# Kernel tuning notes

Measured on AMD Instinct MI355X. Metric: run time of the kernel, lower is better.

Reference implementation:

```python
import jax, jax.numpy as jnp
import numpy as np

B, T_AUDIO, D_IN = 64, 500, 768
H = 1024
NUM_CHARS = 1024  # must equal H: one-hot char embeddings feed the LSTM input
SEQ_LEN = 128


def setup_inputs() -> dict:
    key = jax.random.key(0)
    ks = jax.random.split(key, 16)
    s = 1.0 / np.sqrt(H)
    u = lambda k, shape: jax.random.uniform(k, shape, jnp.float32, -s, s)
    return {
        "audio_features": jax.random.normal(ks[0], (B, T_AUDIO, D_IN), jnp.float32),
        "text_indices": jax.random.randint(ks[1], (B, SEQ_LEN), 0, NUM_CHARS),
        "W_proj": u(ks[2], (H, D_IN)), "b_proj": u(ks[3], (H,)),
        "W_ih0": u(ks[4], (4 * H, H)), "W_hh0": u(ks[5], (4 * H, H)),
        "b_ih0": u(ks[6], (4 * H,)), "b_hh0": u(ks[7], (4 * H,)),
        "W_ih1": u(ks[8], (4 * H, H)), "W_hh1": u(ks[9], (4 * H, H)),
        "b_ih1": u(ks[10], (4 * H,)), "b_hh1": u(ks[11], (4 * H,)),
        "W_out": u(ks[12], (NUM_CHARS, H)), "b_out": u(ks[13], (NUM_CHARS,)),
    }


def _lstm_cell(x, h, c, W_ih, W_hh, b_ih, b_hh):
    # PyTorch gate order: i, f, g, o
    g = x @ W_ih.T + h @ W_hh.T + b_ih + b_hh
    i, f, gg, o = jnp.split(g, 4, axis=-1)
    c = jax.nn.sigmoid(f) * c + jax.nn.sigmoid(i) * jnp.tanh(gg)
    h = jax.nn.sigmoid(o) * jnp.tanh(c)
    return h, c


def reference(audio_features, text_indices, W_proj, b_proj,
              W_ih0, W_hh0, b_ih0, b_hh0,
              W_ih1, W_hh1, b_ih1, b_hh1,
              W_out, b_out):
    # audio encoding: project then mean-pool over time -> [B, H]
    audio_enc = jnp.mean(audio_features @ W_proj.T + b_proj, axis=1)
    seq_len = text_indices.shape[1]
    # teacher-forcing inputs: step 0 = audio encoding, steps 1..L-1 = one-hot of
    # text_indices[:, 1:seq_len-1] (NUM_CHARS == H)
    one_hots = jax.nn.one_hot(text_indices[:, 1:seq_len - 1], NUM_CHARS,
                              dtype=audio_enc.dtype)  # [B, L-1, H]
    xs = jnp.concatenate([audio_enc[:, None, :], one_hots], axis=1)  # [B, L, H]
    xs = jnp.swapaxes(xs, 0, 1)  # [L, B, H]
    z = jnp.zeros((audio_enc.shape[0], H), audio_enc.dtype)

    def step(carry, x):
        h0, c0, h1, c1 = carry
        h0, c0 = _lstm_cell(x, h0, c0, W_ih0, W_hh0, b_ih0, b_hh0)
        h1, c1 = _lstm_cell(h0, h1, c1, W_ih1, W_hh1, b_ih1, b_hh1)
        return (h0, c0, h1, c1), h1

    _, hs = jax.lax.scan(step, (z, z, z, z), xs)  # hs: [L, B, H]
    outs = jnp.swapaxes(hs, 0, 1)  # [B, L, H]
    logits = outs @ W_out.T + b_out  # [B, L, NUM_CHARS]
    return logits
```

## Files before the change

### kernel.cpp

```cpp
#include <hip/hip_runtime.h>
#include <hip/hip_bf16.h>

#define HH     1024
#define BB     64
#define DIN    768
#define TAUD   500
#define LSTEPS 127
#define G4     4096
#define NB     256
#define BHH    (BB*HH)

typedef __attribute__((ext_vector_type(8))) short bf16x8;
typedef __attribute__((ext_vector_type(4))) float f32x4;
typedef unsigned short u16;
typedef unsigned long long u64;

__device__ __forceinline__ u16 f2b(float x){
  __hip_bfloat16 h = __float2bfloat16(x);
  return __builtin_bit_cast(u16, h);
}
__device__ __forceinline__ float b2f(u16 u){
  unsigned int x = ((unsigned int)u) << 16;
  return __builtin_bit_cast(float, x);
}
__device__ __forceinline__ float sig_(float x){ return 1.0f/(1.0f+__expf(-x)); }
__device__ __forceinline__ float tanh_(float x){
  float ax = fabsf(x);
  float e  = __expf(-2.0f*ax);
  float t  = (1.0f-e)/(1.0f+e);
  return x < 0.0f ? -t : t;
}

constexpr size_t O_PACK  = 0;
constexpr size_t O_WG    = O_PACK + (size_t)NB*3*16384*2;
constexpr size_t O_WOHI  = O_WG   + (size_t)NB*16384*2;
constexpr size_t O_WOLO  = O_WOHI + (size_t)HH*HH*2;
constexpr size_t O_B0P   = O_WOLO + (size_t)HH*HH*2;
constexpr size_t O_B1P   = O_B0P  + G4*4;
constexpr size_t O_G0    = O_B1P  + G4*4;
constexpr size_t O_MEAN  = O_G0   + (size_t)BB*HH*4*4;
constexpr size_t O_X0    = O_MEAN + (size_t)BB*DIN*4;
constexpr size_t O_H0    = O_X0   + (size_t)BHH*2;
constexpr size_t O_H1    = O_H0   + (size_t)2*BHH*2;
constexpr size_t O_HS    = O_H1   + (size_t)2*BHH*2;
constexpr size_t O_BAR   = O_HS   + (size_t)LSTEPS*BHH*2;

__global__ void init_kernel(u16* h0, u16* h1, int* bar){
  int i = blockIdx.x*256 + threadIdx.x;
  int st = gridDim.x*256;
  for (int k=i;k<2*BHH;k+=st){ h0[k]=0; h1[k]=0; }
  if (i < 512) bar[i] = 0;
}

__global__ void pool_kernel(const float* __restrict__ audio, float* __restrict__ mean){
  int b = blockIdx.x/3, dc = blockIdx.x%3;
  int d = dc*256 + threadIdx.x;
  const float* p = audio + (size_t)b*TAUD*DIN + d;
  float s = 0.f;
  #pragma unroll 5
  for (int t=0;t<TAUD;++t) s += p[(size_t)t*DIN];
  mean[b*DIN + d] = s*(1.0f/TAUD);
}

__global__ void project_kernel(const float* __restrict__ mean, const float* __restrict__ Wp,
                               const float* __restrict__ bp, u16* __restrict__ x0){
  __shared__ float wrow[DIN];
  __shared__ float part[256];
  int h = blockIdx.x;
  for (int i=threadIdx.x;i<DIN;i+=256) wrow[i] = Wp[(size_t)h*DIN + i];
  __syncthreads();
  int b = threadIdx.x>>2, q = threadIdx.x&3;
  const float* mr = mean + b*DIN + q*192;
  const float* wr = wrow + q*192;
  float s = 0.f;
  #pragma unroll 8
  for (int i=0;i<192;++i) s += mr[i]*wr[i];
  part[threadIdx.x] = s;
  __syncthreads();
  if (q==0){
    float v = part[threadIdx.x]+part[threadIdx.x+1]+part[threadIdx.x+2]+part[threadIdx.x+3] + bp[h];
    x0[b*HH + h] = f2b(v);
  }
}

__global__ void g0_kernel(const float* __restrict__ Wih0, const u16* __restrict__ x0bf,
                          float* __restrict__ G0p){
  __shared__ float wr[4][HH];
  __shared__ float part[256][4];
  int u = blockIdx.x;
  for (int i=threadIdx.x; i<4*HH; i+=256){
    int g = i>>10, k = i&1023;
    wr[g][k] = b2f(f2b(Wih0[(size_t)(u + g*HH)*HH + k]));
  }
  __syncthreads();
  int b = threadIdx.x>>2, q = threadIdx.x&3;
  const u16* xr = x0bf + b*HH + q*256;
  float s0=0,s1=0,s2=0,s3=0;
  for (int k=0;k<256;++k){
    float xv = b2f(xr[k]);
    s0 += xv*wr[0][q*256+k]; s1 += xv*wr[1][q*256+k];
    s2 += xv*wr[2][q*256+k]; s3 += xv*wr[3][q*256+k];
  }
  part[threadIdx.x][0]=s0; part[threadIdx.x][1]=s1;
  part[threadIdx.x][2]=s2; part[threadIdx.x][3]=s3;
  __syncthreads();
  if (threadIdx.x < 64){
    int bb = threadIdx.x;
    #pragma unroll
    for (int g=0;g<4;++g){
      float v = part[bb*4][g]+part[bb*4+1][g]+part[bb*4+2][g]+part[bb*4+3][g];
      G0p[((size_t)bb*HH + u)*4 + g] = v;
    }
  }
}

__global__ void pack_w_kernel(const float* __restrict__ Whh0, const float* __restrict__ Wih1,
                              const float* __restrict__ Whh1, u16* __restrict__ P){
  int bid = blockIdx.x, m = blockIdx.y;
  const float* src = (m==0)? Whh0 : (m==1)? Wih1 : Whh1;
  u16* dst = P + ((size_t)bid*3 + m)*16384;
  for (int e = threadIdx.x; e < 16384; e += 256){
    int r = e&31, col = (e>>5)&15, ktg = e>>9;
    int ng = bid*4 + (col&3) + (col>>2)*HH;
    dst[e] = f2b(src[(size_t)ng*HH + ktg*32 + r]);
  }
}

__global__ void pack_wg_kernel(const float* __restrict__ Wih0, u16* __restrict__ WG){
  int bid = blockIdx.x;
  for (int i = threadIdx.x; i < 16384; i += 256){
    int ch = i>>4, u = (i>>2)&3, g = i&3;
    WG[(size_t)bid*16384 + i] = f2b(Wih0[(size_t)(bid*4 + u + g*HH)*HH + ch]);
  }
}

__global__ void pack_bias_kernel(const float* bih0, const float* bhh0,
                                 const float* bih1, const float* bhh1,
                                 float* B0p, float* B1p){
  int i = blockIdx.x*256 + threadIdx.x;
  if (i < G4){
    int n = (i>>2) + (i&3)*HH;
    B0p[i] = bih0[n]+bhh0[n];
    B1p[i] = bih1[n]+bhh1[n];
  }
}

__global__ void wout_kernel(const float* __restrict__ src, u16* __restrict__ hi,
                            u16* __restrict__ lo, int n){
  int i = blockIdx.x*256+threadIdx.x, st = gridDim.x*256;
  for (;i<n;i+=st){
    float v = src[i];
    u16 h = f2b(v);
    hi[i] = h;
    lo[i] = f2b(v - b2f(h));
  }
}

__device__ __forceinline__ void sysst32(unsigned* p, unsigned v){
  __hip_atomic_store(p, v, __ATOMIC_RELAXED, __HIP_MEMORY_SCOPE_SYSTEM);
}

__device__ __forceinline__ void gridbar(int* bar, int t){
  __syncthreads();
  if (threadIdx.x==0){
    int leaf = blockIdx.x>>4;
    int a = __hip_atomic_fetch_add(&bar[leaf*32], 1, __ATOMIC_RELAXED, __HIP_MEMORY_SCOPE_SYSTEM);
    int r = a - t*16;
    if (r == 15)
      __hip_atomic_fetch_add(&bar[511], 1, __ATOMIC_RELAXED, __HIP_MEMORY_SCOPE_SYSTEM);
    if (r == 0 || r == 15){
      while (__hip_atomic_load(&bar[511], __ATOMIC_RELAXED, __HIP_MEMORY_SCOPE_SYSTEM) < (t+1)*16)
        __builtin_amdgcn_s_sleep(4);
      if (r == 0)
        __hip_atomic_store(&bar[leaf*32+16], t+1, __ATOMIC_RELAXED, __HIP_MEMORY_SCOPE_SYSTEM);
    } else {
      while (__hip_atomic_load(&bar[leaf*32+16], __ATOMIC_RELAXED, __HIP_MEMORY_SCOPE_SYSTEM) < t+1)
        __builtin_amdgcn_s_sleep(4);
    }
    asm volatile("" ::: "memory");
  }
  __syncthreads();
  if (threadIdx.x < 64)
    __builtin_amdgcn_fence(__ATOMIC_ACQUIRE, "agent");
  __syncthreads();
}

__device__ __forceinline__ f32x4 gemmK(const u16* __restrict__ A, const u16* B, f32x4 acc){
  #pragma unroll
  for (int h=0; h<2; ++h){
    bf16x8 af[16];
    #pragma unroll
    for (int i=0;i<16;++i) af[i] = *(const bf16x8*)(A + (h*16+i)*32);
    #pragma unroll
    for (int i=0;i<16;++i)
      acc = __builtin_amdgcn_mfma_f32_16x16x32_bf16(af[i], *(const bf16x8*)(B + (h*16+i)*512), acc, 0,0,0);
  }
  return acc;
}
__device__ __forceinline__ f32x4 gemm2K(const u16* __restrict__ A1, const u16* __restrict__ A2,
                                        const u16* B1, const u16* B2){
  f32x4 a1 = {0,0,0,0}, a2 = {0,0,0,0};
  #pragma unroll
  for (int h=0; h<2; ++h){
    bf16x8 af[16], ag[16];
    #pragma unroll
    for (int i=0;i<16;++i) af[i] = *(const bf16x8*)(A1 + (h*16+i)*32);
    #pragma unroll
    for (int i=0;i<16;++i) ag[i] = *(const bf16x8*)(A2 + (h*16+i)*32);
    #pragma unroll
    for (int i=0;i<16;++i){
      a1 = __builtin_amdgcn_mfma_f32_16x16x32_bf16(af[i], *(const bf16x8*)(B1 + (h*16+i)*512), a1, 0,0,0);
      a2 = __builtin_amdgcn_mfma_f32_16x16x32_bf16(ag[i], *(const bf16x8*)(B2 + (h*16+i)*512), a2, 0,0,0);
    }
  }
  return a1 + a2;
}

__device__ __forceinline__ void xpose(const f32x4 acc, float* gv, int lane){
  const int base = lane & 48, up = (lane>>2)&3, r = lane&3;
  #pragma unroll
  for (int g=0; g<4; ++g){
    int src = base | (g*4 + up);
    float v0 = __shfl(acc[0], src);
    float v1 = __shfl(acc[1], src);
    float v2 = __shfl(acc[2], src);
    float v3 = __shfl(acc[3], src);
    gv[g] = (r==0)? v0 : (r==1)? v1 : (r==2)? v2 : v3;
  }
}

__global__ void __launch_bounds__(256, 1) lstm_kernel(
    const u16* __restrict__ P, const u16* __restrict__ WG,
    const float* __restrict__ B0p, const float* __restrict__ B1p,
    const float* __restrict__ G0p, const int* __restrict__ tix,
    u16* __restrict__ h0bf, u16* __restrict__ h1bf,
    u16* __restrict__ hs, int* __restrict__ bar)
{
  extern __shared__ char smem[];
  u16* Plds = (u16*)smem;
  u16* WGl  = (u16*)(smem + 98304);
  u16* tixl = (u16*)(smem + 98304 + 32768);

  const int tid  = threadIdx.x;
  const int lane = tid&63, mg = tid>>6, quad = lane>>4, colc = lane&15;
  const int bid  = blockIdx.x;

  {
    const bf16x8* gs = (const bf16x8*)(P + (size_t)bid*49152);
    bf16x8* gd = (bf16x8*)Plds;
    #pragma unroll
    for (int i=0;i<24;++i) gd[tid + i*256] = gs[tid + i*256];
    const bf16x8* ws = (const bf16x8*)(WG + (size_t)bid*16384);
    bf16x8* wd = (bf16x8*)WGl;
    #pragma unroll
    for (int i=0;i<8;++i) wd[tid + i*256] = ws[tid + i*256];
    for (int i=tid; i<BB*128; i+=256) tixl[i] = (u16)tix[(i&63)*128 + (i>>6)];
  }

  const int aoff = (mg*16 + colc)*HH + quad*8;
  const int boff = colc*32 + quad*8;
  const u16* B_hh0 = Plds + boff;
  const u16* B_ih1 = Plds + 16384 + boff;
  const u16* B_hh1 = Plds + 2*16384 + boff;

  const int bT = mg*16 + quad*4 + (lane&3);
  const int up = (lane>>2)&3;
  const int ug = bid*4 + up;
  const float4 vb0 = *(const float4*)(B0p + ug*4);
  const float4 vb1 = *(const float4*)(B1p + ug*4);
  float cc0 = 0.f, cc1 = 0.f;
  __syncthreads();

  {
    float4 g0 = *(const float4*)(G0p + ((size_t)bT*HH + ug)*4);
    float gi = g0.x+vb0.x, gf = g0.y+vb0.y, gg = g0.z+vb0.z, go = g0.w+vb0.w;
    cc0 = sig_(gi)*tanh_(gg);
    unsigned hv = f2b(sig_(go)*tanh_(cc0));
    unsigned ov = __shfl_xor(hv, 4);
    if ((lane&4)==0)
      sysst32((unsigned*)(h0bf + (size_t)BHH) + (bT*HH + ug)/2, hv | (ov<<16));
  }

  #pragma unroll 1
  for (int t=0;t<LSTEPS;++t){
    const int cur = t&1, nxt = cur^1;
    gridbar(bar, t);
    {
      f32x4 acc = gemm2K(h0bf + (size_t)nxt*BHH + aoff, h1bf + (size_t)cur*BHH + aoff,
                         B_ih1, B_hh1);
      float gv[4];
      xpose(acc, gv, lane);
      gv[0]+=vb1.x; gv[1]+=vb1.y; gv[2]+=vb1.z; gv[3]+=vb1.w;
      cc1 = sig_(gv[1])*cc1 + sig_(gv[0])*tanh_(gv[2]);
      unsigned hv = f2b(sig_(gv[3])*tanh_(cc1));
      unsigned ov = __shfl_xor(hv, 4);
      if ((lane&4)==0){
        unsigned pk = hv | (ov<<16);
        sysst32((unsigned*)(h1bf + (size_t)nxt*BHH) + (bT*HH + ug)/2, pk);
        sysst32((unsigned*)hs + (((size_t)t*BB + bT)*HH + ug)/2, pk);
      }
    }
    if (t < LSTEPS-1){
      f32x4 z = {0,0,0,0};
      f32x4 acc = gemmK(h0bf + (size_t)nxt*BHH + aoff, B_hh0, z);
      float gv[4];
      xpose(acc, gv, lane);
      int ch = tixl[(t+1)*64 + bT];
      ushort4 wv = *(const ushort4*)(WGl + ch*16 + up*4);
      gv[0]+=vb0.x+b2f(wv.x); gv[1]+=vb0.y+b2f(wv.y);
      gv[2]+=vb0.z+b2f(wv.z); gv[3]+=vb0.w+b2f(wv.w);
      cc0 = sig_(gv[1])*cc0 + sig_(gv[0])*tanh_(gv[2]);
      unsigned hv = f2b(sig_(gv[3])*tanh_(cc0));
      unsigned ov = __shfl_xor(hv, 4);
      if ((lane&4)==0)
        sysst32((unsigned*)(h0bf + (size_t)cur*BHH) + (bT*HH + ug)/2, hv | (ov<<16));
    }
  }
}

__global__ void __launch_bounds__(512) logits_kernel(
    const u16* __restrict__ hs, const u16* __restrict__ Whi, const u16* __restrict__ Wlo,
    const float* __restrict__ bout, float* __restrict__ out)
{
  extern __shared__ u16 bsh[];
  const int tid = threadIdx.x;
  const int w = tid>>6, lane = tid&63, quad = lane>>4, col = lane&15;
  const int mt = blockIdx.x*8 + w;
  const bool active = (mt < (LSTEPS*BB)/16);
  bf16x8 afr[32];
  if (active){
    const u16* ap = hs + (size_t)(mt*16+col)*HH + quad*8;
    #pragma unroll
    for (int kt=0;kt<32;++kt) afr[kt] = *(const bf16x8*)(ap + kt*32);
  }
  const int nt0 = blockIdx.y*16;
  for (int nt=nt0; nt<nt0+16; ++nt){
    __syncthreads();
    #pragma unroll
    for (int i=0;i<8;++i){
      int cid = i*512 + tid;
      int mat = cid>>11;
      int r = (cid>>7)&15, ck = cid&127;
      const u16* src = (mat? Wlo : Whi) + (size_t)(nt*16+r)*HH + ck*8;
      *(bf16x8*)(bsh + mat*16512 + r*1032 + ck*8) = *(const bf16x8*)src;
    }
    __syncthreads();
    if (active){
      f32x4 acc = {0.f,0.f,0.f,0.f};
      const u16* bh = bsh + col*1032 + quad*8;
      const u16* bl = bsh + 16512 + col*1032 + quad*8;
      #pragma unroll 8
      for (int kt=0;kt<32;++kt){
        bf16x8 b1 = *(const bf16x8*)(bh + kt*32);
        acc = __builtin_amdgcn_mfma_f32_16x16x32_bf16(afr[kt], b1, acc, 0,0,0);
        bf16x8 b2 = *(const bf16x8*)(bl + kt*32);
        acc = __builtin_amdgcn_mfma_f32_16x16x32_bf16(afr[kt], b2, acc, 0,0,0);
      }
      float bb = bout[nt*16 + col];
      #pragma unroll
      for (int r=0;r<4;++r){
        int m = mt*16 + quad*4 + r;
        int tt = m>>6, b_ = m&63;
        out[((size_t)b_*LSTEPS + tt)*HH + nt*16 + col] = acc[r] + bb;
      }
    }
  }
}

extern "C" void kernel_launch(void* const* d_in, const int* in_sizes, int n_in,
                              void* d_out, int out_size, void* d_ws, size_t ws_size,
                              hipStream_t stream) {
  const float* audio = (const float*)d_in[0];
  const int*   tix   = (const int*)  d_in[1];
  const float* Wproj = (const float*)d_in[2];
  const float* bproj = (const float*)d_in[3];
  const float* Wih0  = (const float*)d_in[4];
  const float* Whh0  = (const float*)d_in[5];
  const float* bih0  = (const float*)d_in[6];
  const float* bhh0  = (const float*)d_in[7];
  const float* Wih1  = (const float*)d_in[8];
  const float* Whh1  = (const float*)d_in[9];
  const float* bih1  = (const float*)d_in[10];
  const float* bhh1  = (const float*)d_in[11];
  const float* Wout  = (const float*)d_in[12];
  const float* bout  = (const float*)d_in[13];
  float* out = (float*)d_out;

  char* ws = (char*)d_ws;
  u16*   wP    = (u16*)  (ws + O_PACK);
  u16*   wWG   = (u16*)  (ws + O_WG);
  u16*   wWoHi = (u16*)  (ws + O_WOHI);
  u16*   wWoLo = (u16*)  (ws + O_WOLO);
  float* wB0p  = (float*)(ws + O_B0P);
  float* wB1p  = (float*)(ws + O_B1P);
  float* wG0   = (float*)(ws + O_G0);
  float* wMean = (float*)(ws + O_MEAN);
  u16*   wX0   = (u16*)  (ws + O_X0);
  u16*   wH0   = (u16*)  (ws + O_H0);
  u16*   wH1   = (u16*)  (ws + O_H1);
  u16*   wHS   = (u16*)  (ws + O_HS);
  int*   wBar  = (int*)  (ws + O_BAR);

  init_kernel<<<64, 256, 0, stream>>>(wH0, wH1, wBar);
  pool_kernel<<<BB*3, 256, 0, stream>>>(audio, wMean);
  project_kernel<<<HH, 256, 0, stream>>>(wMean, Wproj, bproj, wX0);
  g0_kernel<<<HH, 256, 0, stream>>>(Wih0, wX0, wG0);
  pack_w_kernel<<<dim3(NB,3), 256, 0, stream>>>(Whh0, Wih1, Whh1, wP);
  pack_wg_kernel<<<NB, 256, 0, stream>>>(Wih0, wWG);
  pack_bias_kernel<<<16, 256, 0, stream>>>(bih0, bhh0, bih1, bhh1, wB0p, wB1p);
  wout_kernel<<<512, 256, 0, stream>>>(Wout, wWoHi, wWoLo, HH*HH);
  lstm_kernel<<<NB, 256, 98304 + 32768 + 16384, stream>>>(
      wP, wWG, wB0p, wB1p, wG0, tix, wH0, wH1, wHS, wBar);
  logits_kernel<<<dim3(64,4), 512, 66048, stream>>>(wHS, wWoHi, wWoLo, bout, out);
}
```

Measured before the change: 2.625 ms.

## Use never-reused per-step hidden-state buffers and drop acquire fence from grid barrier

Replaces the double-buffered h0/h1 ping-pong with a full per-timestep history for h0, and reads h1 straight from the hs output history. Because each address is written only once, the acquire fence after the grid barrier is removed on the assumption that stale cache lines cannot exist. The zero-init of the hidden buffers is no longer needed, and step 0 skips the h1 recurrent GEMM. This uses more workspace memory. Correctness now depends on never-written addresses not being held in non-coherent caches without a fence.

```diff
diff --git a/kernel.cpp b/kernel.cpp
--- a/kernel.cpp
+++ b/kernel.cpp
@@ -40,16 +40,12 @@
 constexpr size_t O_G0    = O_B1P  + G4*4;
 constexpr size_t O_MEAN  = O_G0   + (size_t)BB*HH*4*4;
 constexpr size_t O_X0    = O_MEAN + (size_t)BB*DIN*4;
-constexpr size_t O_H0    = O_X0   + (size_t)BHH*2;
-constexpr size_t O_H1    = O_H0   + (size_t)2*BHH*2;
-constexpr size_t O_HS    = O_H1   + (size_t)2*BHH*2;
+constexpr size_t O_H0R   = O_X0   + (size_t)BHH*2;
+constexpr size_t O_HS    = O_H0R  + (size_t)LSTEPS*BHH*2;
 constexpr size_t O_BAR   = O_HS   + (size_t)LSTEPS*BHH*2;
 
-__global__ void init_kernel(u16* h0, u16* h1, int* bar){
-  int i = blockIdx.x*256 + threadIdx.x;
-  int st = gridDim.x*256;
-  for (int k=i;k<2*BHH;k+=st){ h0[k]=0; h1[k]=0; }
-  if (i < 512) bar[i] = 0;
+__global__ void init_kernel(int* bar){
+  if (threadIdx.x < 512) bar[threadIdx.x] = 0;
 }
 
 __global__ void pool_kernel(const float* __restrict__ audio, float* __restrict__ mean){
@@ -180,9 +176,6 @@
     asm volatile("" ::: "memory");
   }
   __syncthreads();
-  if (threadIdx.x < 64)
-    __builtin_amdgcn_fence(__ATOMIC_ACQUIRE, "agent");
-  __syncthreads();
 }
 
 __device__ __forceinline__ f32x4 gemmK(const u16* __restrict__ A, const u16* B, f32x4 acc){
@@ -233,8 +226,7 @@
     const u16* __restrict__ P, const u16* __restrict__ WG,
     const float* __restrict__ B0p, const float* __restrict__ B1p,
     const float* __restrict__ G0p, const int* __restrict__ tix,
-    u16* __restrict__ h0bf, u16* __restrict__ h1bf,
-    u16* __restrict__ hs, int* __restrict__ bar)
+    u16* __restrict__ h0r, u16* __restrict__ hs, int* __restrict__ bar)
 {
   extern __shared__ char smem[];
   u16* Plds = (u16*)smem;
@@ -273,36 +265,38 @@
 
   {
     float4 g0 = *(const float4*)(G0p + ((size_t)bT*HH + ug)*4);
-    float gi = g0.x+vb0.x, gf = g0.y+vb0.y, gg = g0.z+vb0.z, go = g0.w+vb0.w;
+    float gi = g0.x+vb0.x, gg = g0.z+vb0.z, go = g0.w+vb0.w;
     cc0 = sig_(gi)*tanh_(gg);
     unsigned hv = f2b(sig_(go)*tanh_(cc0));
     unsigned ov = __shfl_xor(hv, 4);
     if ((lane&4)==0)
-      sysst32((unsigned*)(h0bf + (size_t)BHH) + (bT*HH + ug)/2, hv | (ov<<16));
+      sysst32((unsigned*)h0r + (bT*HH + ug)/2, hv | (ov<<16));
   }
 
   #pragma unroll 1
   for (int t=0;t<LSTEPS;++t){
-    const int cur = t&1, nxt = cur^1;
     gridbar(bar, t);
+    const u16* A1 = h0r + (size_t)t*BHH + aoff;
     {
-      f32x4 acc = gemm2K(h0bf + (size_t)nxt*BHH + aoff, h1bf + (size_t)cur*BHH + aoff,
-                         B_ih1, B_hh1);
+      f32x4 acc;
+      if (t==0){
+        f32x4 z = {0,0,0,0};
+        acc = gemmK(A1, B_ih1, z);
+      } else {
+        acc = gemm2K(A1, hs + (size_t)(t-1)*BHH + aoff, B_ih1, B_hh1);
+      }
       float gv[4];
       xpose(acc, gv, lane);
       gv[0]+=vb1.x; gv[1]+=vb1.y; gv[2]+=vb1.z; gv[3]+=vb1.w;
       cc1 = sig_(gv[1])*cc1 + sig_(gv[0])*tanh_(gv[2]);
       unsigned hv = f2b(sig_(gv[3])*tanh_(cc1));
       unsigned ov = __shfl_xor(hv, 4);
-      if ((lane&4)==0){
-        unsigned pk = hv | (ov<<16);
-        sysst32((unsigned*)(h1bf + (size_t)nxt*BHH) + (bT*HH + ug)/2, pk);
-        sysst32((unsigned*)hs + (((size_t)t*BB + bT)*HH + ug)/2, pk);
-      }
+      if ((lane&4)==0)
+        sysst32((unsigned*)hs + (((size_t)t*BB + bT)*HH + ug)/2, hv | (ov<<16));
     }
     if (t < LSTEPS-1){
       f32x4 z = {0,0,0,0};
-      f32x4 acc = gemmK(h0bf + (size_t)nxt*BHH + aoff, B_hh0, z);
+      f32x4 acc = gemmK(A1, B_hh0, z);
       float gv[4];
       xpose(acc, gv, lane);
       int ch = tixl[(t+1)*64 + bT];
@@ -313,7 +307,7 @@
       unsigned hv = f2b(sig_(gv[3])*tanh_(cc0));
       unsigned ov = __shfl_xor(hv, 4);
       if ((lane&4)==0)
-        sysst32((unsigned*)(h0bf + (size_t)cur*BHH) + (bT*HH + ug)/2, hv | (ov<<16));
+        sysst32((unsigned*)(h0r + (size_t)(t+1)*BHH) + (bT*HH + ug)/2, hv | (ov<<16));
     }
   }
 }
@@ -396,12 +390,11 @@
   float* wG0   = (float*)(ws + O_G0);
   float* wMean = (float*)(ws + O_MEAN);
   u16*   wX0   = (u16*)  (ws + O_X0);
-  u16*   wH0   = (u16*)  (ws + O_H0);
-  u16*   wH1   = (u16*)  (ws + O_H1);
+  u16*   wH0R  = (u16*)  (ws + O_H0R);
   u16*   wHS   = (u16*)  (ws + O_HS);
   int*   wBar  = (int*)  (ws + O_BAR);
 
-  init_kernel<<<64, 256, 0, stream>>>(wH0, wH1, wBar);
+  init_kernel<<<1, 512, 0, stream>>>(wBar);
   pool_kernel<<<BB*3, 256, 0, stream>>>(audio, wMean);
   project_kernel<<<HH, 256, 0, stream>>>(wMean, Wproj, bproj, wX0);
   g0_kernel<<<HH, 256, 0, stream>>>(Wih0, wX0, wG0);
@@ -410,6 +403,6 @@
   pack_bias_kernel<<<16, 256, 0, stream>>>(bih0, bhh0, bih1, bhh1, wB0p, wB1p);
   wout_kernel<<<512, 256, 0, stream>>>(Wout, wWoHi, wWoLo, HH*HH);
   lstm_kernel<<<NB, 256, 98304 + 32768 + 16384, stream>>>(
-      wP, wWG, wB0p, wB1p, wG0, tix, wH0, wH1, wHS, wBar);
+      wP, wWG, wB0p, wB1p, wG0, tix, wH0R, wHS, wBar);
   logits_kernel<<<dim3(64,4), 512, 66048, stream>>>(wHS, wWoHi, wWoLo, bout, out);
 }
```

Result: faster. 2.438 ms (-7.2%).
